# Kernel optimization log

Measured on AMD Instinct MI355X. Metric: run time of the kernel, lower is better.

The kernel has to match this reference:

```python
import jax, jax.numpy as jnp
import numpy as np

H_DIM = 512
FF_DIM = 2048
N_HEAD = 4
N_BLOCK = 3
N_TOKEN = 128
B, S = 8, 1024
LN_EPS = 1e-5


def _layernorm(x, g, b):
    mu = jnp.mean(x, axis=-1, keepdims=True)
    var = jnp.mean(jnp.square(x - mu), axis=-1, keepdims=True)
    return (x - mu) * jax.lax.rsqrt(var + LN_EPS) * g + b


def setup_inputs() -> dict:
    key = jax.random.key(0)
    ks = jax.random.split(key, 20)
    sc = 0.02
    inp = {
        'input_ids': jax.random.randint(ks[0], (B, S), 0, N_TOKEN, dtype=jnp.int32),
        'attention_mask': jnp.ones((B, S), dtype=jnp.int32),
        'emb': jax.random.uniform(ks[1], (N_TOKEN, H_DIM), dtype=jnp.float32),
        'wq': jax.random.normal(ks[2], (N_BLOCK, N_HEAD, H_DIM, H_DIM), dtype=jnp.float32) * sc,
        'wk': jax.random.normal(ks[3], (N_BLOCK, N_HEAD, H_DIM, H_DIM), dtype=jnp.float32) * sc,
        'wv': jax.random.normal(ks[4], (N_BLOCK, N_HEAD, H_DIM, H_DIM), dtype=jnp.float32) * sc,
        'wo_w': jax.random.normal(ks[5], (N_BLOCK, N_HEAD * H_DIM, H_DIM), dtype=jnp.float32) * sc,
        'wo_b': jnp.zeros((N_BLOCK, H_DIM), dtype=jnp.float32),
        'ln1_g': jnp.ones((N_BLOCK, H_DIM), dtype=jnp.float32),
        'ln1_b': jnp.zeros((N_BLOCK, H_DIM), dtype=jnp.float32),
        'ff1_w': jax.random.normal(ks[6], (N_BLOCK, FF_DIM, H_DIM), dtype=jnp.float32) * sc,
        'ff1_b': jnp.zeros((N_BLOCK, FF_DIM), dtype=jnp.float32),
        'ff2_w': jax.random.normal(ks[7], (N_BLOCK, H_DIM, FF_DIM), dtype=jnp.float32) * sc,
        'ff2_b': jnp.zeros((N_BLOCK, H_DIM), dtype=jnp.float32),
        'ln2_g': jnp.ones((N_BLOCK, H_DIM), dtype=jnp.float32),
        'ln2_b': jnp.zeros((N_BLOCK, H_DIM), dtype=jnp.float32),
        'lm_w': jax.random.normal(ks[8], (H_DIM, N_TOKEN), dtype=jnp.float32) * sc,
    }
    return inp


def reference(emb, wq, wk, wv, wo_w, wo_b, ln1_g, ln1_b, ff1_w, ff1_b,
              ff2_w, ff2_b, ln2_g, ln2_b, lm_w, input_ids, attention_mask):
    mask_f = attention_mask.astype(jnp.float32)          # [B,S]
    valid = attention_mask != 0                          # [B,S]

    # Embedding lookup
    x = emb[input_ids]                                   # [B,S,H]

    # Positional encoding: positions assigned sequentially to valid tokens;
    # both even and odd feature slots get the SAME sin value (per source).
    pos = jnp.cumsum(mask_f, axis=-1) - 1.0              # [B,S]
    div = jnp.exp(jnp.arange(0, H_DIM, 2, dtype=jnp.float32) * (-jnp.log(10000.0) / H_DIM))  # [H/2]
    s = jnp.sin(pos[..., None] * div)                    # [B,S,H/2]
    pos_enc = jnp.repeat(s, 2, axis=-1) * mask_f[..., None]
    x = x + pos_enc

    # Allowed attention: causal (key <= query) AND query valid AND key valid
    rows = jnp.arange(S)
    causal = rows[None, :, None] >= rows[None, None, :]  # [1,S,S] (query>=key)
    allowed = causal & valid[:, :, None] & valid[:, None, :]  # [B,S,S]
    neg_inf = jnp.float32(-jnp.inf)
    scale = jnp.sqrt(jnp.float32(H_DIM))

    for l in range(N_BLOCK):
        # Per-head full-width attention (each head uses full H_DIM)
        q = jnp.einsum('bsh,nhd->bnsd', x, wq[l])
        k = jnp.einsum('bsh,nhd->bnsd', x, wk[l])
        v = jnp.einsum('bsh,nhd->bnsd', x, wv[l])
        scores = jnp.einsum('bnsd,bntd->bnst', q, k) / scale      # [B,N,S,S]
        scores = jnp.where(allowed[:, None], scores, neg_inf)
        att = jax.nn.softmax(scores, axis=-1)
        att = jnp.where(jnp.isnan(att), 0.0, att)                  # NaN rows -> 0
        o = jnp.einsum('bnst,bntd->bnsd', att, v)                  # [B,N,S,H]
        o = jnp.transpose(o, (0, 2, 1, 3)).reshape(B, S, N_HEAD * H_DIM)
        mh = o @ wo_w[l] + wo_b[l]
        x = _layernorm(x + mh, ln1_g[l], ln1_b[l])
        # Conv1d with kernel 1 == pointwise linear
        ff = jax.nn.relu(jnp.einsum('bsh,fh->bsf', x, ff1_w[l]) + ff1_b[l])
        ff = jnp.einsum('bsf,hf->bsh', ff, ff2_w[l]) + ff2_b[l]
        x = _layernorm(x + ff, ln2_g[l], ln2_b[l])

    return x @ lm_w                                       # [B,S,N_TOKEN]
```

## Files before the change

kernel.cpp:

```cpp
#include <hip/hip_runtime.h>
#include <hip/hip_bf16.h>

#define S_LEN 1024
#define BATCH 8
#define HD 512
#define FFD 2048
#define NHEAD 4
#define NBLK 3
#define NTOK 128

typedef __bf16 bf16_t;
typedef __bf16 bf16x4_t __attribute__((ext_vector_type(4)));
typedef __bf16 bf16x8_t __attribute__((ext_vector_type(8)));
typedef float f32x4_t __attribute__((ext_vector_type(4)));

typedef __attribute__((address_space(3))) uint32_t lds_u32;
typedef __attribute__((address_space(1))) uint32_t glb_u32;

template<int NI>
__device__ __forceinline__ void ldsread(const bf16_t* __restrict__ buf, int row0,
                                        int fr, int fg, int sw, bf16x8_t (&dst)[NI][2]) {
  #pragma unroll
  for (int i = 0; i < NI; ++i)
    #pragma unroll
    for (int ks = 0; ks < 2; ++ks)
      dst[i][ks] = *(const bf16x8_t*)&buf[(row0 + i*16 + fr)*64 + (((ks*4 + fg) ^ sw) << 3)];
}

template<int IB, int JB>
__device__ __forceinline__ void mquad(f32x4_t (&acc)[8][4],
                                      const bf16x8_t (&af)[4][2], const bf16x8_t (&bf)[2][2]) {
  #pragma unroll
  for (int ks = 0; ks < 2; ++ks)
    #pragma unroll
    for (int i = 0; i < 4; ++i)
      #pragma unroll
      for (int j = 0; j < 2; ++j)
        acc[IB+i][JB+j] = __builtin_amdgcn_mfma_f32_16x16x32_bf16(af[i][ks], bf[j][ks], acc[IB+i][JB+j], 0, 0, 0);
}

template<bool OUT_BF16, bool BIAS, bool RELU, bool TRI, bool CKLIM, bool SB, bool SM>
__global__ __launch_bounds__(512, 2)
void gemm256_kernel(const bf16_t* __restrict__ A,
                    const bf16_t* __restrict__ Bt,
                    const float* __restrict__ bias,
                    void* __restrict__ Cv,
                    int M, int N, int K,
                    int lda, int ldb, int ldc,
                    long long sA, long long sB, int bshift, long long sBias,
                    int zshift, long long sC_hi, long long sC_lo,
                    int msub_shift, long long msub_stride,
                    float alpha,
                    const int* __restrict__ kmask, float* __restrict__ lpart, int pair0)
{
  const int zb = blockIdx.z;
  int m0, n0, tri_ni = 0;
  if (TRI) {
    const int idx = blockIdx.x;
    int mi = (int)((sqrtf(8.f * idx + 1.f) - 1.f) * 0.5f);
    while ((mi + 1) * (mi + 2) / 2 <= idx) ++mi;
    while (mi * (mi + 1) / 2 > idx) --mi;
    m0 = mi * 256;
    tri_ni = idx - mi * (mi + 1) / 2;
    n0 = tri_ni * 256;
  } else {
    m0 = blockIdx.x * 256;
    n0 = blockIdx.y * 256;
  }
  int kend = K;
  if (CKLIM) { int ke = m0 + 256; kend = ke < K ? ke : K; }
  const int nt = kend >> 6;

  const bf16_t* Az = A + (long long)zb * sA;
  const bf16_t* Bz = Bt + (long long)(zb >> bshift) * sB;
  const long long coff = ((long long)(zb >> zshift)) * sC_hi
                       + ((long long)(zb & ((1 << zshift) - 1))) * sC_lo;

  __shared__ __align__(16) bf16_t As[SB ? 1 : 2][256 * 64];
  __shared__ __align__(16) bf16_t Bs[SB ? 1 : 2][256 * 64];

  const int tid = threadIdx.x;
  const int lane = tid & 63;
  const int w = tid >> 6;
  const int wm = (w >> 2) * 128;
  const int wn = (w & 3) * 64;
  const int fr = lane & 15;
  const int fg = lane >> 4;
  const int sw = fr & 7;

  const int srow = tid >> 3;
  const int scol8 = tid & 7;
  const int gswz = ((scol8 ^ (srow & 7)) << 3);

  f32x4_t acc[8][4];
  #pragma unroll
  for (int i = 0; i < 8; ++i)
    #pragma unroll
    for (int j = 0; j < 4; ++j)
      acc[i][j] = (f32x4_t){0.f, 0.f, 0.f, 0.f};

  const bf16_t* gA0 = Az + (long long)(m0 + srow) * lda + gswz;
  const bf16_t* gB0 = Bz + (long long)(n0 + srow) * ldb + gswz;

  auto stage_half = [&](int buf, int kt, int h) {
    if (h < 2) {
      const bf16_t* g = gA0 + (long long)(h * 128) * lda + (kt << 6);
      bf16_t* l = &As[buf][(h*128 + srow) * 64 + (scol8 << 3)];
      __builtin_amdgcn_global_load_lds((const glb_u32*)g, (lds_u32*)l, 16, 0, 0);
      __builtin_amdgcn_global_load_lds((const glb_u32*)(g + 64LL*lda), (lds_u32*)(l + 64*64), 16, 0, 0);
    } else {
      const int hh = h - 2;
      const bf16_t* g = gB0 + (long long)(hh * 128) * ldb + (kt << 6);
      bf16_t* l = &Bs[buf][(hh*128 + srow) * 64 + (scol8 << 3)];
      __builtin_amdgcn_global_load_lds((const glb_u32*)g, (lds_u32*)l, 16, 0, 0);
      __builtin_amdgcn_global_load_lds((const glb_u32*)(g + 64LL*ldb), (lds_u32*)(l + 64*64), 16, 0, 0);
    }
  };

  if constexpr (SB) {
    for (int t = 0; t < nt; ++t) {
      stage_half(0, t, 0); stage_half(0, t, 1); stage_half(0, t, 2); stage_half(0, t, 3);
      __syncthreads();
      bf16x8_t a0[4][2], a1[4][2], b0[2][2], b1[2][2];
      ldsread<4>(&As[0][0], wm, fr, fg, sw, a0);
      ldsread<2>(&Bs[0][0], wn, fr, fg, sw, b0);
      mquad<0, 0>(acc, a0, b0);
      ldsread<4>(&As[0][0], wm + 64, fr, fg, sw, a1);
      ldsread<2>(&Bs[0][0], wn + 32, fr, fg, sw, b1);
      mquad<4, 2>(acc, a1, b1);
      mquad<0, 2>(acc, a0, b1);
      mquad<4, 0>(acc, a1, b0);
      __syncthreads();
    }
  } else {
    stage_half(0, 0, 0); stage_half(0, 0, 1); stage_half(0, 0, 2); stage_half(0, 0, 3);
    if (nt > 1) { stage_half(1, 1, 0); stage_half(1, 1, 1); }
    if (nt > 1) asm volatile("s_waitcnt vmcnt(4)" ::: "memory");
    else        asm volatile("s_waitcnt vmcnt(0)" ::: "memory");
    __builtin_amdgcn_s_barrier();
    __builtin_amdgcn_sched_barrier(0);

    for (int t = 0; t < nt; ++t) {
      const int cur = t & 1;
      const bf16_t* Ac = &As[cur][0];
      const bf16_t* Bc = &Bs[cur][0];
      bf16x8_t a0[4][2], a1[4][2], b0[2][2], b1[2][2];

      ldsread<4>(Ac, wm, fr, fg, sw, a0);
      ldsread<2>(Bc, wn, fr, fg, sw, b0);
      if (t + 1 < nt) stage_half(cur ^ 1, t + 1, 2);
      mquad<0, 0>(acc, a0, b0);
      ldsread<4>(Ac, wm + 64, fr, fg, sw, a1);
      ldsread<2>(Bc, wn + 32, fr, fg, sw, b1);
      if (t + 1 < nt) stage_half(cur ^ 1, t + 1, 3);
      mquad<4, 2>(acc, a1, b1);

      __builtin_amdgcn_s_barrier();
      __builtin_amdgcn_sched_barrier(0);

      if (t + 2 < nt) stage_half(cur, t + 2, 0);
      mquad<0, 2>(acc, a0, b1);
      if (t + 2 < nt) {
        stage_half(cur, t + 2, 1);
        asm volatile("s_waitcnt vmcnt(4)" ::: "memory");
      } else {
        asm volatile("s_waitcnt vmcnt(0)" ::: "memory");
      }
      mquad<4, 0>(acc, a1, b0);

      __builtin_amdgcn_s_barrier();
      __builtin_amdgcn_sched_barrier(0);
    }
  }

  float* lsum = nullptr;
  int km[4];
  if constexpr (SM) {
    lsum = (float*)&As[0][0];
    __syncthreads();
    if (tid < 256) lsum[tid] = 0.f;
    const int* mrow = kmask + (long long)((pair0 + zb) >> 2) * S_LEN;
    #pragma unroll
    for (int j = 0; j < 4; ++j) km[j] = mrow[n0 + wn + j*16 + fr];
    __syncthreads();
  }

  #pragma unroll
  for (int i = 0; i < 8; ++i) {
    #pragma unroll
    for (int e = 0; e < 4; ++e) {
      const int row = m0 + wm + i*16 + fg*4 + e;
      const long long ro = coff
        + ((long long)(row >> msub_shift)) * msub_stride
        + (long long)(row & ((1 << msub_shift) - 1)) * (long long)ldc;
      float rsum = 0.f;
      #pragma unroll
      for (int j = 0; j < 4; ++j) {
        const int col = n0 + wn + j*16 + fr;
        float v = acc[i][j][e] * alpha;
        if constexpr (SM) {
          const float pv = (col <= row && km[j]) ? __expf(v) : 0.f;
          rsum += pv;
          ((bf16_t*)Cv)[ro + col] = (bf16_t)pv;
        } else {
          if (BIAS) v += bias[(long long)zb * sBias + col];
          if (RELU) v = v > 0.f ? v : 0.f;
          if (OUT_BF16) ((bf16_t*)Cv)[ro + col] = (bf16_t)v;
          else          ((float*)Cv)[ro + col]  = v;
        }
      }
      if constexpr (SM) {
        rsum += __shfl_xor(rsum, 1);
        rsum += __shfl_xor(rsum, 2);
        rsum += __shfl_xor(rsum, 4);
        rsum += __shfl_xor(rsum, 8);
        if (fr == 0) atomicAdd(&lsum[wm + i*16 + fg*4 + e], rsum);
      }
    }
  }

  if constexpr (SM) {
    __syncthreads();
    if (tid < 256)
      lpart[((long long)zb * S_LEN + m0 + tid) * 4 + tri_ni] = lsum[tid];
  }
}

template<bool OUT_BF16, bool BIAS, bool RELU, bool CSKIP, bool CKLIM, bool NORM>
__global__ __launch_bounds__(256, 2)
void gemm_bt_kernel(const bf16_t* __restrict__ A,
                    const bf16_t* __restrict__ Bt,
                    const float* __restrict__ bias,
                    void* __restrict__ Cv,
                    int M, int N, int K,
                    int lda, int ldb, int ldc,
                    long long sA, long long sB, long long sBias,
                    int zshift, long long sC_hi, long long sC_lo,
                    int msub_shift, long long msub_stride,
                    float alpha)
{
  const int zb = blockIdx.z;
  const int m0 = blockIdx.x * 128;
  const int n0 = blockIdx.y * 128;
  if (CSKIP && n0 > m0 + 127) return;
  int kend = K;
  if (CKLIM) { int ke = m0 + 128; kend = ke < K ? ke : K; }

  const bf16_t* Az = A + (long long)zb * sA;
  const bf16_t* Bz = Bt + (long long)zb * sB;
  const long long coff = ((long long)(zb >> zshift)) * sC_hi
                       + ((long long)(zb & ((1 << zshift) - 1))) * sC_lo;

  __shared__ __align__(16) bf16_t As[128 * 64];
  __shared__ __align__(16) bf16_t Bs[128 * 64];

  const int tid = threadIdx.x;
  const int wv = tid >> 6;
  const int lane = tid & 63;
  const int wm = (wv >> 1) * 64;
  const int wn = (wv & 1) * 64;
  const int fr = lane & 15;
  const int fg = lane >> 4;
  const int sw = fr & 7;

  f32x4_t acc[4][4];
  #pragma unroll
  for (int i = 0; i < 4; ++i)
    #pragma unroll
    for (int j = 0; j < 4; ++j)
      acc[i][j] = (f32x4_t){0.f, 0.f, 0.f, 0.f};

  const bf16_t* ga = Az + (long long)(m0 + (wv << 5) + (lane >> 3)) * lda
                   + (((lane & 7) ^ (lane >> 3)) << 3);
  const bf16_t* gb = Bz + (long long)(n0 + (wv << 5) + (lane >> 3)) * ldb
                   + (((lane & 7) ^ (lane >> 3)) << 3);

  for (int k0 = 0; k0 < kend; k0 += 64) {
    #pragma unroll
    for (int s = 0; s < 4; ++s) {
      __builtin_amdgcn_global_load_lds(
        (const glb_u32*)(ga + (long long)s * 8 * lda + k0),
        (lds_u32*)(As + (wv * 4 + s) * 512), 16, 0, 0);
      __builtin_amdgcn_global_load_lds(
        (const glb_u32*)(gb + (long long)s * 8 * ldb + k0),
        (lds_u32*)(Bs + (wv * 4 + s) * 512), 16, 0, 0);
    }
    __syncthreads();
    #pragma unroll
    for (int kc = 0; kc < 2; ++kc) {
      const int ca = ((kc * 4 + fg) ^ sw) << 3;
      bf16x8_t af[4], bfr[4];
      #pragma unroll
      for (int i = 0; i < 4; ++i)
        af[i] = *(const bf16x8_t*)&As[(wm + i*16 + fr) * 64 + ca];
      #pragma unroll
      for (int j = 0; j < 4; ++j)
        bfr[j] = *(const bf16x8_t*)&Bs[(wn + j*16 + fr) * 64 + ca];
      #pragma unroll
      for (int i = 0; i < 4; ++i)
        #pragma unroll
        for (int j = 0; j < 4; ++j)
          acc[i][j] = __builtin_amdgcn_mfma_f32_16x16x32_bf16(af[i], bfr[j], acc[i][j], 0, 0, 0);
    }
    __syncthreads();
  }

  #pragma unroll
  for (int i = 0; i < 4; ++i) {
    #pragma unroll
    for (int e = 0; e < 4; ++e) {
      const int row = m0 + wm + i*16 + fg*4 + e;
      const long long ro = coff
        + ((long long)(row >> msub_shift)) * msub_stride
        + (long long)(row & ((1 << msub_shift) - 1)) * (long long)ldc;
      float rn = 1.f;
      if (NORM) rn = bias[(long long)zb * sBias + row];
      #pragma unroll
      for (int j = 0; j < 4; ++j) {
        const int col = n0 + wn + j*16 + fr;
        float v = acc[i][j][e] * alpha;
        if (BIAS) v += bias[(long long)zb * sBias + col];
        if (NORM) v *= rn;
        if (RELU) v = v > 0.f ? v : 0.f;
        if (OUT_BF16) ((bf16_t*)Cv)[ro + col] = (bf16_t)v;
        else          ((float*)Cv)[ro + col]  = v;
      }
    }
  }
}

__global__ void linv_kernel(const float* __restrict__ lpart, const int* __restrict__ mask,
                            float* __restrict__ linv, int pair0)
{
  const int idx = blockIdx.x * 256 + threadIdx.x;
  const int pr = idx >> 10;
  const int row = idx & (S_LEN - 1);
  const int b = (pair0 + pr) >> 2;
  const int nlim = (row >> 8) + 1;
  const float* lp = lpart + (long long)idx * 4;
  float l = 0.f;
  for (int n = 0; n < nlim; ++n) l += lp[n];
  linv[idx] = (mask[b * S_LEN + row] != 0 && l > 0.f) ? 1.f / l : 0.f;
}

template<typename TIN>
__global__ void transpose_kernel(const TIN* __restrict__ in, bf16_t* __restrict__ out,
                                 int R, int C, long long sIn, long long sOut)
{
  __shared__ float tile[32][33];
  const long long zi = (long long)blockIdx.z * sIn;
  const long long zo = (long long)blockIdx.z * sOut;
  const int c0 = blockIdx.x * 32, r0 = blockIdx.y * 32;
  const int tx = threadIdx.x, ty = threadIdx.y;
  #pragma unroll
  for (int i = 0; i < 4; ++i) {
    int r = r0 + ty + i*8;
    tile[ty + i*8][tx] = (float)in[zi + (long long)r * C + c0 + tx];
  }
  __syncthreads();
  #pragma unroll
  for (int i = 0; i < 4; ++i) {
    int c = c0 + ty + i*8;
    out[zo + (long long)c * R + r0 + tx] = (bf16_t)tile[tx][ty + i*8];
  }
}

__global__ void convert2_kernel(const float* __restrict__ a, const float* __restrict__ b,
                                bf16_t* __restrict__ out, long long n)
{
  long long i = (long long)blockIdx.x * blockDim.x + threadIdx.x;
  long long stride = (long long)gridDim.x * blockDim.x;
  for (; i < 2*n; i += stride)
    out[i] = (bf16_t)(i < n ? a[i] : b[i - n]);
}

__global__ void fill_kernel(float* __restrict__ out, long long n, float v)
{
  long long i = (long long)blockIdx.x * blockDim.x + threadIdx.x;
  long long stride = (long long)gridDim.x * blockDim.x;
  for (; i < n; i += stride) out[i] = v;
}

__global__ void pos_kernel(const int* __restrict__ mask, float* __restrict__ pos)
{
  __shared__ float scn[S_LEN];
  const int b = blockIdx.x, t = threadIdx.x;
  scn[t] = (float)(mask[b * S_LEN + t] != 0);
  __syncthreads();
  for (int off = 1; off < S_LEN; off <<= 1) {
    float add = (t >= off) ? scn[t - off] : 0.f;
    __syncthreads();
    scn[t] += add;
    __syncthreads();
  }
  pos[b * S_LEN + t] = scn[t] - 1.0f;
}

__global__ void embed_kernel(const int* __restrict__ ids, const int* __restrict__ mask,
                             const float* __restrict__ pos, const float* __restrict__ emb,
                             float* __restrict__ x, bf16_t* __restrict__ xb)
{
  const int idx = blockIdx.x * 256 + threadIdx.x;
  const int i = idx & 255;
  const int bs = idx >> 8;
  const int id = ids[bs];
  const float m = (float)(mask[bs] != 0);
  const float p = pos[bs];
  const float dv = __expf(-(float)(2 * i) * (9.210340371976184f / (float)HD));
  const float sv = __sinf(p * dv) * m;
  const float e0 = emb[id * HD + 2*i], e1 = emb[id * HD + 2*i + 1];
  const float x0 = e0 + sv, x1 = e1 + sv;
  x[(long long)bs * HD + 2*i]     = x0;
  x[(long long)bs * HD + 2*i + 1] = x1;
  xb[(long long)bs * HD + 2*i]     = (bf16_t)x0;
  xb[(long long)bs * HD + 2*i + 1] = (bf16_t)x1;
}

__global__ void ln_kernel(float* __restrict__ x, const float* __restrict__ tparts,
                          int ns, long long pstride,
                          const float* __restrict__ bias,
                          const float* __restrict__ g, const float* __restrict__ b,
                          bf16_t* __restrict__ xb)
{
  const int lane = threadIdx.x & 63;
  const long long row = (long long)blockIdx.x * 4 + (threadIdx.x >> 6);
  const int e0 = lane * 8;
  const long long base = row * HD + e0;

  float4 xa = *(const float4*)&x[base];
  float4 xc = *(const float4*)&x[base + 4];
  float4 ba = *(const float4*)&bias[e0];
  float4 bc = *(const float4*)&bias[e0 + 4];
  float v[8] = {xa.x+ba.x, xa.y+ba.y, xa.z+ba.z, xa.w+ba.w,
                xc.x+bc.x, xc.y+bc.y, xc.z+bc.z, xc.w+bc.w};
  for (int i = 0; i < ns; ++i) {
    float4 p0 = *(const float4*)&tparts[i*pstride + base];
    float4 p1 = *(const float4*)&tparts[i*pstride + base + 4];
    v[0]+=p0.x; v[1]+=p0.y; v[2]+=p0.z; v[3]+=p0.w;
    v[4]+=p1.x; v[5]+=p1.y; v[6]+=p1.z; v[7]+=p1.w;
  }
  float s = 0.f;
  #pragma unroll
  for (int j = 0; j < 8; ++j) s += v[j];
  #pragma unroll
  for (int o = 32; o; o >>= 1) s += __shfl_xor(s, o);
  const float mu = s * (1.f / (float)HD);
  float q = 0.f;
  #pragma unroll
  for (int j = 0; j < 8; ++j) { v[j] -= mu; q += v[j]*v[j]; }
  #pragma unroll
  for (int o = 32; o; o >>= 1) q += __shfl_xor(q, o);
  const float inv = rsqrtf(q * (1.f / (float)HD) + 1e-5f);

  float4 ga4 = *(const float4*)&g[e0];
  float4 gc4 = *(const float4*)&g[e0 + 4];
  float4 bb4 = *(const float4*)&b[e0];
  float4 bd4 = *(const float4*)&b[e0 + 4];
  float y[8] = {v[0]*inv*ga4.x+bb4.x, v[1]*inv*ga4.y+bb4.y, v[2]*inv*ga4.z+bb4.z, v[3]*inv*ga4.w+bb4.w,
                v[4]*inv*gc4.x+bd4.x, v[5]*inv*gc4.y+bd4.y, v[6]*inv*gc4.z+bd4.z, v[7]*inv*gc4.w+bd4.w};
  *(float4*)&x[base]     = (float4){y[0],y[1],y[2],y[3]};
  *(float4*)&x[base + 4] = (float4){y[4],y[5],y[6],y[7]};
  bf16x8_t yb;
  #pragma unroll
  for (int j = 0; j < 8; ++j) yb[j] = (bf16_t)y[j];
  *(bf16x8_t*)&xb[base] = yb;
}

extern "C" void kernel_launch(void* const* d_in, const int* in_sizes, int n_in,
                              void* d_out, int out_size, void* d_ws, size_t ws_size,
                              hipStream_t stream)
{
  (void)in_sizes; (void)n_in;
  const int*   ids   = (const int*)d_in[0];
  const int*   amask = (const int*)d_in[1];
  const float* emb   = (const float*)d_in[2];
  const float* wq    = (const float*)d_in[3];
  const float* wk    = (const float*)d_in[4];
  const float* wv    = (const float*)d_in[5];
  const float* wo_w  = (const float*)d_in[6];
  const float* wo_b  = (const float*)d_in[7];
  const float* ln1_g = (const float*)d_in[8];
  const float* ln1_b = (const float*)d_in[9];
  const float* ff1_w = (const float*)d_in[10];
  const float* ff1_b = (const float*)d_in[11];
  const float* ff2_w = (const float*)d_in[12];
  const float* ff2_b = (const float*)d_in[13];
  const float* ln2_g = (const float*)d_in[14];
  const float* ln2_b = (const float*)d_in[15];
  const float* lm_w  = (const float*)d_in[16];

  const long long MROW = (long long)BATCH * S_LEN;
  const size_t MBc = 1ull << 20;
  char* p = (char*)d_ws;
  auto alloc = [&](size_t bytes) { char* r = p; p += (bytes + 255) & ~(size_t)255; return r; };

  float*  x     = (float*) alloc(MROW * HD * 4);
  bf16_t* xb    = (bf16_t*)alloc(MROW * HD * 2);
  bf16_t* ob    = (bf16_t*)alloc(MROW * (NHEAD*HD) * 2);
  bf16_t* wqkb  = (bf16_t*)alloc(8LL * HD * HD * 2);
  bf16_t* wvT   = (bf16_t*)alloc(4LL * HD * HD * 2);
  bf16_t* Gt    = (bf16_t*)alloc(4LL * HD * HD * 2);
  bf16_t* woT   = (bf16_t*)alloc((long long)HD * FFD * 2);
  bf16_t* wff1  = (bf16_t*)alloc((long long)FFD * HD * 2);
  bf16_t* wff2  = (bf16_t*)alloc((long long)HD * FFD * 2);
  bf16_t* lmT   = (bf16_t*)alloc((long long)NTOK * HD * 2);
  float*  pos   = (float*) alloc(MROW * 4);
  float*  lpart = (float*) alloc(32LL * S_LEN * 4 * 4);
  float*  linv  = (float*) alloc(32LL * S_LEN * 4);

  const size_t used = (size_t)(p - (char*)d_ws);
  const size_t rem  = ws_size > used ? ws_size - used : 0;

  int P = 0, SK = 2;
  if      (rem >= 128 * MBc) { P = 32; SK = 4; }
  else if (rem >= 64 * MBc)  { P = 8;  SK = 2; }
  if (P == 0) {
    fill_kernel<<<1024, 256, 0, stream>>>((float*)d_out, (long long)out_size,
                                          (float)(ws_size >> 20));
    return;
  }

  char* A = p;
  const long long pairE = (long long)S_LEN * HD;
  bf16_t* qc  = (bf16_t*)A;
  bf16_t* vTc = qc  + (long long)P * pairE;
  bf16_t* scb = vTc + (long long)P * pairE;
  float*  tmp = (float*)A;
  bf16_t* ffb = (bf16_t*)(A + (size_t)SK * 16 * MBc);

  const dim3 tb(32, 8);
  transpose_kernel<float><<<dim3(4,16,1), tb, 0, stream>>>(lm_w, lmT, HD, NTOK, 0, 0);
  pos_kernel<<<BATCH, S_LEN, 0, stream>>>(amask, pos);
  embed_kernel<<<8192, 256, 0, stream>>>(ids, amask, pos, emb, x, xb);

  const int nch = 32 / P;
  const int bpc = P / NHEAD;

  for (int l = 0; l < NBLK; ++l) {
    convert2_kernel<<<2048, 256, 0, stream>>>(
      wq + (long long)l*NHEAD*HD*HD, wk + (long long)l*NHEAD*HD*HD, wqkb, 4LL*HD*HD);
    transpose_kernel<float><<<dim3(16,16,4), tb, 0, stream>>>(
      wv + (long long)l*NHEAD*HD*HD, wvT, HD, HD, (long long)HD*HD, (long long)HD*HD);
    transpose_kernel<float><<<dim3(16,64,1), tb, 0, stream>>>(
      wo_w + (long long)l*FFD*HD, woT, FFD, HD, 0, 0);
    convert2_kernel<<<2048, 256, 0, stream>>>(
      ff1_w + (long long)l*FFD*HD, ff2_w + (long long)l*HD*FFD, wff1, (long long)FFD*HD);
    gemm_bt_kernel<true,false,false,false,false,false><<<dim3(4,4,4),256,0,stream>>>(
      wqkb + 4LL*HD*HD, wqkb, nullptr, Gt,
      HD, HD, HD, HD, HD, HD,
      (long long)HD*HD, (long long)HD*HD, 0,
      30, 0, (long long)HD*HD,
      30, 0, 1.f);

    for (int c = 0; c < nch; ++c) {
      const int b0 = c * bpc;
      const int pair0 = b0 * NHEAD;
      const int Mch = bpc * S_LEN;

      gemm256_kernel<true,false,false,false,false,false,false><<<dim3(Mch/256,2,4),512,0,stream>>>(
        xb + (long long)b0*S_LEN*HD, Gt, nullptr, qc, Mch, HD, HD, HD, HD, HD,
        0, (long long)HD*HD, 0, 0,
        2, 0, pairE,
        10, (long long)NHEAD*pairE, 1.f, nullptr, nullptr, 0);

      gemm256_kernel<true,false,false,false,false,false,false><<<dim3(8,4,bpc),512,0,stream>>>(
        wvT, xb + (long long)b0*S_LEN*HD, nullptr, vTc,
        2048, S_LEN, HD, HD, HD, S_LEN,
        0, (long long)S_LEN*HD, 0, 0,
        0, (long long)NHEAD*HD*S_LEN, 0,
        9, (long long)HD*S_LEN, 1.f, nullptr, nullptr, 0);

      gemm256_kernel<true,false,false,true,false,true,true><<<dim3(10,1,P),512,0,stream>>>(
        qc, xb + (long long)b0*S_LEN*HD, nullptr, scb,
        S_LEN, S_LEN, HD, HD, HD, S_LEN,
        pairE, (long long)S_LEN*HD, 2, 0,
        30, 0, (long long)S_LEN*S_LEN,
        30, 0, 0.044194173824159216f, amask, lpart, pair0);

      linv_kernel<<<P*S_LEN/256,256,0,stream>>>(lpart, amask, linv, pair0);

      gemm_bt_kernel<true,false,false,false,true,true><<<dim3(8,4,P),256,0,stream>>>(
        scb, vTc, linv,
        ob + (long long)b0*S_LEN*(NHEAD*HD),
        S_LEN, HD, S_LEN, S_LEN, S_LEN, NHEAD*HD,
        (long long)S_LEN*S_LEN, (long long)HD*S_LEN, S_LEN,
        2, (long long)S_LEN*NHEAD*HD, HD,
        30, 0, 1.f);
    }

    gemm256_kernel<false,false,false,false,false,false,false><<<dim3(32,2,SK),512,0,stream>>>(
      ob, woT, nullptr, tmp,
      (int)MROW, HD, (NHEAD*HD)/SK, NHEAD*HD, NHEAD*HD, HD,
      (NHEAD*HD)/SK, (NHEAD*HD)/SK, 0, 0,
      0, (long long)MROW*HD, 0,
      30, 0, 1.f, nullptr, nullptr, 0);
    ln_kernel<<<2048,256,0,stream>>>(x, tmp, SK, (long long)MROW*HD,
                                     wo_b + l*HD, ln1_g + l*HD, ln1_b + l*HD, xb);

    gemm256_kernel<true,true,true,false,false,false,false><<<dim3(32,8,1),512,0,stream>>>(
      xb, wff1, ff1_b + l*FFD, ffb,
      (int)MROW, FFD, HD, HD, HD, FFD,
      0, 0, 0, 0, 30, 0, 0, 30, 0, 1.f, nullptr, nullptr, 0);
    gemm256_kernel<false,false,false,false,false,false,false><<<dim3(32,2,SK),512,0,stream>>>(
      ffb, wff2, nullptr, tmp,
      (int)MROW, HD, FFD/SK, FFD, FFD, HD,
      FFD/SK, FFD/SK, 0, 0,
      0, (long long)MROW*HD, 0,
      30, 0, 1.f, nullptr, nullptr, 0);
    ln_kernel<<<2048,256,0,stream>>>(x, tmp, SK, (long long)MROW*HD,
                                     ff2_b + l*HD, ln2_g + l*HD, ln2_b + l*HD, xb);
  }

  gemm_bt_kernel<false,false,false,false,false,false><<<dim3(64,1,1),256,0,stream>>>(
    xb, lmT, nullptr, (float*)d_out,
    (int)MROW, NTOK, HD, HD, HD, NTOK,
    0, 0, 0, 30, 0, 0, 30, 0, 1.f);
}
```

Measured before the change: 911.0 us.

## Route attention PV GEMM through 256-tile kernel with row-normalization epilogue

The attention P·V product moves from the older gemm_bt kernel onto the double-buffered 256x256 MFMA kernel, which gains a NORM epilogue that scales each output row by its inverse softmax sum. The QK score kernel drops its single-buffer mode and uses the pipelined double-buffered loop. It also writes per-wave partial row sums straight to a wider lpart buffer, replacing the LDS atomic reduction and its extra barriers. SM/NORM variants get launch bounds allowing one block per CU, which may cut occupancy, and the PV grid shrinks to fewer, larger tiles with causal K limiting.

```diff
diff --git a/kernel.cpp b/kernel.cpp
--- a/kernel.cpp
+++ b/kernel.cpp
@@ -39,8 +39,8 @@
         acc[IB+i][JB+j] = __builtin_amdgcn_mfma_f32_16x16x32_bf16(af[i][ks], bf[j][ks], acc[IB+i][JB+j], 0, 0, 0);
 }
 
-template<bool OUT_BF16, bool BIAS, bool RELU, bool TRI, bool CKLIM, bool SB, bool SM>
-__global__ __launch_bounds__(512, 2)
+template<bool OUT_BF16, bool BIAS, bool RELU, bool TRI, bool CKLIM, bool SM, bool NORM>
+__global__ __launch_bounds__(512, (SM || NORM) ? 1 : 2)
 void gemm256_kernel(const bf16_t* __restrict__ A,
                     const bf16_t* __restrict__ Bt,
                     const float* __restrict__ bias,
@@ -76,8 +76,8 @@
   const long long coff = ((long long)(zb >> zshift)) * sC_hi
                        + ((long long)(zb & ((1 << zshift) - 1))) * sC_lo;
 
-  __shared__ __align__(16) bf16_t As[SB ? 1 : 2][256 * 64];
-  __shared__ __align__(16) bf16_t Bs[SB ? 1 : 2][256 * 64];
+  __shared__ __align__(16) bf16_t As[2][256 * 64];
+  __shared__ __align__(16) bf16_t Bs[2][256 * 64];
 
   const int tid = threadIdx.x;
   const int lane = tid & 63;
@@ -117,72 +117,51 @@
     }
   };
 
-  if constexpr (SB) {
-    for (int t = 0; t < nt; ++t) {
-      stage_half(0, t, 0); stage_half(0, t, 1); stage_half(0, t, 2); stage_half(0, t, 3);
-      __syncthreads();
-      bf16x8_t a0[4][2], a1[4][2], b0[2][2], b1[2][2];
-      ldsread<4>(&As[0][0], wm, fr, fg, sw, a0);
-      ldsread<2>(&Bs[0][0], wn, fr, fg, sw, b0);
-      mquad<0, 0>(acc, a0, b0);
-      ldsread<4>(&As[0][0], wm + 64, fr, fg, sw, a1);
-      ldsread<2>(&Bs[0][0], wn + 32, fr, fg, sw, b1);
-      mquad<4, 2>(acc, a1, b1);
-      mquad<0, 2>(acc, a0, b1);
-      mquad<4, 0>(acc, a1, b0);
-      __syncthreads();
-    }
-  } else {
-    stage_half(0, 0, 0); stage_half(0, 0, 1); stage_half(0, 0, 2); stage_half(0, 0, 3);
-    if (nt > 1) { stage_half(1, 1, 0); stage_half(1, 1, 1); }
-    if (nt > 1) asm volatile("s_waitcnt vmcnt(4)" ::: "memory");
-    else        asm volatile("s_waitcnt vmcnt(0)" ::: "memory");
+  stage_half(0, 0, 0); stage_half(0, 0, 1); stage_half(0, 0, 2); stage_half(0, 0, 3);
+  if (nt > 1) { stage_half(1, 1, 0); stage_half(1, 1, 1); }
+  if (nt > 1) asm volatile("s_waitcnt vmcnt(4)" ::: "memory");
+  else        asm volatile("s_waitcnt vmcnt(0)" ::: "memory");
+  __builtin_amdgcn_s_barrier();
+  __builtin_amdgcn_sched_barrier(0);
+
+  for (int t = 0; t < nt; ++t) {
+    const int cur = t & 1;
+    const bf16_t* Ac = &As[cur][0];
+    const bf16_t* Bc = &Bs[cur][0];
+    bf16x8_t a0[4][2], a1[4][2], b0[2][2], b1[2][2];
+
+    ldsread<4>(Ac, wm, fr, fg, sw, a0);
+    ldsread<2>(Bc, wn, fr, fg, sw, b0);
+    if (t + 1 < nt) stage_half(cur ^ 1, t + 1, 2);
+    mquad<0, 0>(acc, a0, b0);
+    ldsread<4>(Ac, wm + 64, fr, fg, sw, a1);
+    ldsread<2>(Bc, wn + 32, fr, fg, sw, b1);
+    if (t + 1 < nt) stage_half(cur ^ 1, t + 1, 3);
+    mquad<4, 2>(acc, a1, b1);
+
     __builtin_amdgcn_s_barrier();
     __builtin_amdgcn_sched_barrier(0);
 
-    for (int t = 0; t < nt; ++t) {
-      const int cur = t & 1;
-      const bf16_t* Ac = &As[cur][0];
-      const bf16_t* Bc = &Bs[cur][0];
-      bf16x8_t a0[4][2], a1[4][2], b0[2][2], b1[2][2];
-
-      ldsread<4>(Ac, wm, fr, fg, sw, a0);
-      ldsread<2>(Bc, wn, fr, fg, sw, b0);
-      if (t + 1 < nt) stage_half(cur ^ 1, t + 1, 2);
-      mquad<0, 0>(acc, a0, b0);
-      ldsread<4>(Ac, wm + 64, fr, fg, sw, a1);
-      ldsread<2>(Bc, wn + 32, fr, fg, sw, b1);
-      if (t + 1 < nt) stage_half(cur ^ 1, t + 1, 3);
-      mquad<4, 2>(acc, a1, b1);
-
-      __builtin_amdgcn_s_barrier();
-      __builtin_amdgcn_sched_barrier(0);
-
-      if (t + 2 < nt) stage_half(cur, t + 2, 0);
-      mquad<0, 2>(acc, a0, b1);
-      if (t + 2 < nt) {
-        stage_half(cur, t + 2, 1);
-        asm volatile("s_waitcnt vmcnt(4)" ::: "memory");
-      } else {
-        asm volatile("s_waitcnt vmcnt(0)" ::: "memory");
-      }
-      mquad<4, 0>(acc, a1, b0);
-
-      __builtin_amdgcn_s_barrier();
-      __builtin_amdgcn_sched_barrier(0);
-    }
-  }
-
-  float* lsum = nullptr;
+    if (t + 2 < nt) stage_half(cur, t + 2, 0);
+    mquad<0, 2>(acc, a0, b1);
+    if (t + 2 < nt) {
+      stage_half(cur, t + 2, 1);
+      asm volatile("s_waitcnt vmcnt(4)" ::: "memory");
+    } else {
+      asm volatile("s_waitcnt vmcnt(0)" ::: "memory");
+    }
+    mquad<4, 0>(acc, a1, b0);
+
+    __builtin_amdgcn_s_barrier();
+    __builtin_amdgcn_sched_barrier(0);
+  }
+  __builtin_amdgcn_sched_barrier(0);
+
   int km[4];
   if constexpr (SM) {
-    lsum = (float*)&As[0][0];
-    __syncthreads();
-    if (tid < 256) lsum[tid] = 0.f;
     const int* mrow = kmask + (long long)((pair0 + zb) >> 2) * S_LEN;
     #pragma unroll
     for (int j = 0; j < 4; ++j) km[j] = mrow[n0 + wn + j*16 + fr];
-    __syncthreads();
   }
 
   #pragma unroll
@@ -194,6 +173,8 @@
         + ((long long)(row >> msub_shift)) * msub_stride
         + (long long)(row & ((1 << msub_shift) - 1)) * (long long)ldc;
       float rsum = 0.f;
+      float rn = 1.f;
+      if (NORM) rn = bias[(long long)zb * sBias + row];
       #pragma unroll
       for (int j = 0; j < 4; ++j) {
         const int col = n0 + wn + j*16 + fr;
@@ -204,6 +185,7 @@
           ((bf16_t*)Cv)[ro + col] = (bf16_t)pv;
         } else {
           if (BIAS) v += bias[(long long)zb * sBias + col];
+          if (NORM) v *= rn;
           if (RELU) v = v > 0.f ? v : 0.f;
           if (OUT_BF16) ((bf16_t*)Cv)[ro + col] = (bf16_t)v;
           else          ((float*)Cv)[ro + col]  = v;
@@ -214,15 +196,10 @@
         rsum += __shfl_xor(rsum, 2);
         rsum += __shfl_xor(rsum, 4);
         rsum += __shfl_xor(rsum, 8);
-        if (fr == 0) atomicAdd(&lsum[wm + i*16 + fg*4 + e], rsum);
+        if (fr == 0)
+          lpart[(((long long)zb << 10) + row) * 16 + tri_ni * 4 + (w & 3)] = rsum;
       }
     }
-  }
-
-  if constexpr (SM) {
-    __syncthreads();
-    if (tid < 256)
-      lpart[((long long)zb * S_LEN + m0 + tid) * 4 + tri_ni] = lsum[tid];
   }
 }
 
@@ -336,10 +313,10 @@
   const int pr = idx >> 10;
   const int row = idx & (S_LEN - 1);
   const int b = (pair0 + pr) >> 2;
-  const int nlim = (row >> 8) + 1;
-  const float* lp = lpart + (long long)idx * 4;
+  const int cnt = ((row >> 8) + 1) * 4;
+  const float* lp = lpart + (long long)idx * 16;
   float l = 0.f;
-  for (int n = 0; n < nlim; ++n) l += lp[n];
+  for (int n = 0; n < cnt; ++n) l += lp[n];
   linv[idx] = (mask[b * S_LEN + row] != 0 && l > 0.f) ? 1.f / l : 0.f;
 }
 
@@ -505,7 +482,7 @@
   bf16_t* wff2  = (bf16_t*)alloc((long long)HD * FFD * 2);
   bf16_t* lmT   = (bf16_t*)alloc((long long)NTOK * HD * 2);
   float*  pos   = (float*) alloc(MROW * 4);
-  float*  lpart = (float*) alloc(32LL * S_LEN * 4 * 4);
+  float*  lpart = (float*) alloc(32LL * S_LEN * 16 * 4);
   float*  linv  = (float*) alloc(32LL * S_LEN * 4);
 
   const size_t used = (size_t)(p - (char*)d_ws);
@@ -570,7 +547,7 @@
         0, (long long)NHEAD*HD*S_LEN, 0,
         9, (long long)HD*S_LEN, 1.f, nullptr, nullptr, 0);
 
-      gemm256_kernel<true,false,false,true,false,true,true><<<dim3(10,1,P),512,0,stream>>>(
+      gemm256_kernel<true,false,false,true,false,true,false><<<dim3(10,1,P),512,0,stream>>>(
         qc, xb + (long long)b0*S_LEN*HD, nullptr, scb,
         S_LEN, S_LEN, HD, HD, HD, S_LEN,
         pairE, (long long)S_LEN*HD, 2, 0,
@@ -579,13 +556,13 @@
 
       linv_kernel<<<P*S_LEN/256,256,0,stream>>>(lpart, amask, linv, pair0);
 
-      gemm_bt_kernel<true,false,false,false,true,true><<<dim3(8,4,P),256,0,stream>>>(
+      gemm256_kernel<true,false,false,false,true,false,true><<<dim3(4,2,P),512,0,stream>>>(
         scb, vTc, linv,
         ob + (long long)b0*S_LEN*(NHEAD*HD),
         S_LEN, HD, S_LEN, S_LEN, S_LEN, NHEAD*HD,
-        (long long)S_LEN*S_LEN, (long long)HD*S_LEN, S_LEN,
+        (long long)S_LEN*S_LEN, (long long)HD*S_LEN, 0, S_LEN,
         2, (long long)S_LEN*NHEAD*HD, HD,
-        30, 0, 1.f);
+        30, 0, 1.f, nullptr, nullptr, 0);
     }
 
     gemm256_kernel<false,false,false,false,false,false,false><<<dim3(32,2,SK),512,0,stream>>>(
```

Result: slower. 940.9 us (+3.3%).
